# Optimization experiments

Hardware: AMD Instinct MI355X
Metric: run time of the kernel (lower is better)

Reference implementation:

```python
import jax, jax.numpy as jnp
import numpy as np

B, S, D, H, M = 2, 2048, 1024, 16, 4096
DH = D // H
EPS = 1e-6  # flax LayerNorm default
THETA = 10000.0


def layer_norm(x, scale, bias):
    m = jnp.mean(x, axis=-1, keepdims=True)
    v = jnp.var(x, axis=-1, keepdims=True)
    return (x - m) * jax.lax.rsqrt(v + EPS) * scale + bias


def apply_rope(xq, xk):
    # xq, xk: [B, S, H, DH]; rotate consecutive pairs as complex numbers
    half = DH // 2
    freqs = 1.0 / THETA ** (jnp.arange(0, DH, 2)[:half].astype(jnp.float32) / DH)
    t = jnp.arange(S, dtype=jnp.float32)
    ang = jnp.outer(t, freqs)                      # [S, half]
    cos = jnp.cos(ang)[None, :, None, :]           # [1, S, 1, half]
    sin = jnp.sin(ang)[None, :, None, :]

    def rot(x):
        xr = x.astype(jnp.float32).reshape(*x.shape[:-1], half, 2)
        a, b = xr[..., 0], xr[..., 1]
        out = jnp.stack((a * cos - b * sin, a * sin + b * cos), axis=-1)
        return out.reshape(*x.shape).astype(jnp.float32)

    return rot(xq), rot(xk)


def setup_inputs() -> dict:
    key = jax.random.key(0)
    ks = jax.random.split(key, 12)
    sd = 1.0 / np.sqrt(D)
    return {
        "x": jax.random.normal(ks[0], (B, S, D), jnp.float32),
        "ln1_s": jnp.ones((D,), jnp.float32),
        "ln1_b": jnp.zeros((D,), jnp.float32),
        "wk": jax.random.normal(ks[1], (D, D), jnp.float32) * sd,
        "wq": jax.random.normal(ks[2], (D, D), jnp.float32) * sd,
        "wv": jax.random.normal(ks[3], (D, D), jnp.float32) * sd,
        "wo": jax.random.normal(ks[4], (D, D), jnp.float32) * sd,
        "ln2_s": jnp.ones((D,), jnp.float32),
        "ln2_b": jnp.zeros((D,), jnp.float32),
        "w1": jax.random.normal(ks[5], (D, M), jnp.float32) * sd,
        "b1": jnp.zeros((M,), jnp.float32),
        "w2": jax.random.normal(ks[6], (M, D), jnp.float32) * (1.0 / np.sqrt(M)),
        "b2": jnp.zeros((D,), jnp.float32),
    }


def reference(x, ln1_s, ln1_b, wk, wq, wv, wo, ln2_s, ln2_b, w1, b1, w2, b2):
    h = layer_norm(x, ln1_s, ln1_b)
    xk = (h @ wk).reshape(B, S, H, DH)
    xq = (h @ wq).reshape(B, S, H, DH)
    xv = (h @ wv).reshape(B, S, H, DH)
    xq, xk = apply_rope(xq, xk)
    # scores: [B, H, S, S]
    scores = jnp.einsum("bqhd,bkhd->bhqk", xq, xk) / jnp.sqrt(jnp.float32(DH))
    attn = jax.nn.softmax(scores, axis=-1)
    ctx = jnp.einsum("bhqk,bkhd->bqhd", attn, xv).reshape(B, S, D)
    attn_out = ctx @ wo
    mlp_in = attn_out + x
    h2 = layer_norm(mlp_in, ln2_s, ln2_b)
    h2 = jax.nn.gelu(h2 @ w1 + b1)  # approximate gelu (jax default, matches source)
    h2 = h2 @ w2 + b2
    return h2 + mlp_in
```

## Files before the change

kernel.cpp:

```cpp
#include <hip/hip_runtime.h>
#include <stdint.h>

#define B_ 2
#define S_ 2048
#define D_ 1024
#define H_ 16
#define DH_ 64
#define M_ 4096
#define BS_ 4096

typedef __attribute__((ext_vector_type(8))) short short8;
typedef __attribute__((ext_vector_type(4))) float f32x4;
typedef __attribute__((ext_vector_type(16))) float f32x16;

static __device__ __forceinline__ unsigned short f2bf(float f) {
  unsigned u = __float_as_uint(f);
  u += 0x7fffu + ((u >> 16) & 1u);
  return (unsigned short)(u >> 16);
}
static __device__ __forceinline__ float bf2f(unsigned short s) {
  return __uint_as_float(((unsigned)s) << 16);
}
static __device__ __forceinline__ f32x4 MFMA16(short8 a, short8 b, f32x4 c) {
  return __builtin_amdgcn_mfma_f32_16x16x32_bf16(a, b, c, 0, 0, 0);
}
static __device__ __forceinline__ f32x16 MFMA32(short8 a, short8 b, f32x16 c) {
  return __builtin_amdgcn_mfma_f32_32x32x16_bf16(a, b, c, 0, 0, 0);
}
static __device__ __forceinline__ void gload_lds16(const void* g, void* l) {
  __builtin_amdgcn_global_load_lds(
      (const __attribute__((address_space(1))) unsigned int*)g,
      (__attribute__((address_space(3))) unsigned int*)l, 16, 0, 0);
}
static __device__ __forceinline__ unsigned cvtpk_bf16(float lo, float hi) {
  unsigned r;
  asm("v_cvt_pk_bf16_f32 %0, %1, %2" : "=v"(r) : "v"(lo), "v"(hi));
  return r;
}
static __device__ __forceinline__ float gelu_f(float x) {
  float u = 0.7978845608028654f * (x + 0.044715f * x * x * x);
  return 0.5f * x * (1.0f + tanhf(u));
}

__global__ __launch_bounds__(256) void tcast_kernel(const float* __restrict__ in,
                                                    unsigned short* __restrict__ out,
                                                    int R, int C) {
  __shared__ float tile[32][33];
  int tx = threadIdx.x & 31, ty = threadIdx.x >> 5;
  int r0 = blockIdx.y * 32, c0 = blockIdx.x * 32;
#pragma unroll
  for (int i = 0; i < 4; ++i)
    tile[ty + i * 8][tx] = in[(size_t)(r0 + ty + i * 8) * C + c0 + tx];
  __syncthreads();
#pragma unroll
  for (int i = 0; i < 4; ++i)
    out[(size_t)(c0 + ty + i * 8) * R + r0 + tx] = f2bf(tile[tx][ty + i * 8]);
}

__global__ __launch_bounds__(256) void ln_kernel(const float* __restrict__ x,
                                                 const float* __restrict__ sc,
                                                 const float* __restrict__ bi,
                                                 unsigned short* __restrict__ out) {
  int row = blockIdx.x;
  int t = threadIdx.x;
  float4 v = ((const float4*)(x + (size_t)row * D_))[t];
  float s1 = v.x + v.y + v.z + v.w;
  float s2 = v.x * v.x + v.y * v.y + v.z * v.z + v.w * v.w;
#pragma unroll
  for (int m = 1; m < 64; m <<= 1) {
    s1 += __shfl_xor(s1, m);
    s2 += __shfl_xor(s2, m);
  }
  __shared__ float red[8];
  int w = t >> 6, l = t & 63;
  if (l == 0) { red[w] = s1; red[4 + w] = s2; }
  __syncthreads();
  s1 = red[0] + red[1] + red[2] + red[3];
  s2 = red[4] + red[5] + red[6] + red[7];
  float mean = s1 * (1.0f / D_);
  float var = s2 * (1.0f / D_) - mean * mean;
  float rstd = rsqrtf(var + 1e-6f);
  float4 scv = ((const float4*)sc)[t];
  float4 biv = ((const float4*)bi)[t];
  ushort4 o;
  o.x = f2bf((v.x - mean) * rstd * scv.x + biv.x);
  o.y = f2bf((v.y - mean) * rstd * scv.y + biv.y);
  o.z = f2bf((v.z - mean) * rstd * scv.z + biv.z);
  o.w = f2bf((v.w - mean) * rstd * scv.w + biv.w);
  ((ushort4*)out)[(size_t)row * (D_ / 4) + t] = o;
}

__global__ __launch_bounds__(256) void rope_kernel(unsigned short* __restrict__ t_,
                                                   float qscale) {
  size_t idx = (size_t)blockIdx.x * 256 + threadIdx.x;
  int c = (int)(idx & 7);
  size_t rowi = idx >> 3;
  int s = (int)(rowi & (S_ - 1));
  unsigned short* p = t_ + rowi * DH_ + c * 8;
  short8 v = *(const short8*)p;
  unsigned short o[8];
#pragma unroll
  for (int i = 0; i < 4; ++i) {
    int pi = c * 4 + i;
    float freq = exp2f(-(float)pi * 0.4152410118609203f);
    float ang = (float)s * freq;
    float sn, cs;
    sincosf(ang, &sn, &cs);
    float a = bf2f((unsigned short)v[2 * i]);
    float b = bf2f((unsigned short)v[2 * i + 1]);
    o[2 * i] = f2bf((a * cs - b * sn) * qscale);
    o[2 * i + 1] = f2bf((a * sn + b * cs) * qscale);
  }
  short8 ov;
#pragma unroll
  for (int i = 0; i < 8; ++i) ov[i] = (short)o[i];
  *(short8*)p = ov;
}

__global__ __launch_bounds__(256) void attn_kernel(const unsigned short* __restrict__ q,
                                                   const unsigned short* __restrict__ k,
                                                   const unsigned short* __restrict__ vt,
                                                   unsigned short* __restrict__ ctx) {
  __shared__ char smem[49152];
  const int tid = threadIdx.x, w = tid >> 6, l = tid & 63;
  const int lo = l & 31, hi = l >> 5;
  char* Ps = smem + 32768 + w * 4096;
  int flat = blockIdx.y * 16 + blockIdx.x;
  int swz = (flat & 7) * 64 + (flat >> 3);
  const int bh = swz >> 4;
  const int b = bh >> 4, h = bh & 15;
  const int q0 = (swz & 15) * 128 + w * 32;

  const unsigned short* qbase = q + ((size_t)bh * S_ + q0 + lo) * DH_ + hi * 8;
  short8 qf[4];
#pragma unroll
  for (int c = 0; c < 4; ++c) qf[c] = *(const short8*)(qbase + c * 16);

  const unsigned short* kb = k + (size_t)bh * S_ * DH_;
  const unsigned short* vb = vt + (size_t)bh * DH_ * S_;

  short8 onesB;
#pragma unroll
  for (int i = 0; i < 8; ++i) onesB[i] = (short)0x3F80;

  f32x16 o0, o1, lac;
#pragma unroll
  for (int i = 0; i < 16; ++i) { o0[i] = 0.f; o1[i] = 0.f; lac[i] = 0.f; }

#define STAGE_KV(buf, kt)                                                        \
  {                                                                              \
    char* Ks_ = smem + (buf) * 16384;                                            \
    char* Vs_ = Ks_ + 8192;                                                      \
    _Pragma("unroll") for (int i = 0; i < 2; ++i) {                              \
      int slot = i * 256 + tid;                                                  \
      int r = slot >> 3, pc = slot & 7;                                          \
      int sc_ = pc ^ (r & 7);                                                    \
      gload_lds16(kb + (size_t)((kt) + r) * DH_ + sc_ * 8,                       \
                  Ks_ + (i * 4096 + w * 1024));                                  \
      gload_lds16(vb + (size_t)r * S_ + (kt) + sc_ * 8,                          \
                  Vs_ + (i * 4096 + w * 1024));                                  \
    }                                                                            \
  }

  STAGE_KV(0, 0);
  asm volatile("s_waitcnt vmcnt(0)" ::: "memory");
  __builtin_amdgcn_s_barrier();

  for (int t = 0; t < S_ / 64; ++t) {
    int buf = t & 1;
    if (t + 1 < S_ / 64) STAGE_KV(buf ^ 1, (t + 1) * 64);
    char* Ks = smem + buf * 16384;
    char* Vs = Ks + 8192;

#pragma unroll
    for (int kt2 = 0; kt2 < 2; ++kt2) {
      f32x16 z;
#pragma unroll
      for (int i = 0; i < 16; ++i) z[i] = 0.f;
      __builtin_amdgcn_s_setprio(1);
#pragma unroll
      for (int c = 0; c < 4; ++c) {
        int r = kt2 * 32 + lo;
        short8 kf = *(const short8*)(Ks + r * 128 + (((hi + 2 * c) ^ (r & 7)) << 4));
        z = MFMA32(kf, qf[c], z);
      }
      __builtin_amdgcn_s_setprio(0);
      unsigned pk[8];
#pragma unroll
      for (int e = 0; e < 8; ++e)
        pk[e] = cvtpk_bf16(exp2f(z[2 * e]), exp2f(z[2 * e + 1]));
#pragma unroll
      for (int s2 = 0; s2 < 4; ++s2) {
        uint2 dd;
        dd.x = pk[2 * s2];
        dd.y = pk[2 * s2 + 1];
        int slot = kt2 * 4 + s2;
        *(uint2*)(Ps + lo * 128 + ((slot ^ (lo & 7)) << 4) + hi * 8) = dd;
      }
    }

    __builtin_amdgcn_s_setprio(1);
#pragma unroll
    for (int c = 0; c < 4; ++c) {
      short8 pa = *(const short8*)(Ps + lo * 128 + (((2 * c + hi) ^ (lo & 7)) << 4));
      lac = MFMA32(pa, onesB, lac);
      int r0v = lo, r1v = 32 + lo;
      short8 vf0 = *(const short8*)(Vs + r0v * 128 + (((2 * c + hi) ^ (r0v & 7)) << 4));
      short8 vf1 = *(const short8*)(Vs + r1v * 128 + (((2 * c + hi) ^ (r1v & 7)) << 4));
      o0 = MFMA32(pa, vf0, o0);
      o1 = MFMA32(pa, vf1, o1);
    }
    __builtin_amdgcn_s_setprio(0);
    asm volatile("s_waitcnt vmcnt(0)" ::: "memory");
    __builtin_amdgcn_s_barrier();
  }

#pragma unroll
  for (int r = 0; r < 16; ++r) {
    float rl = 1.0f / lac[r];
    int srow = q0 + (r & 3) + 8 * (r >> 2) + 4 * hi;
    unsigned short* cp = ctx + ((size_t)(b * S_) + srow) * D_ + h * DH_ + lo;
    cp[0] = f2bf(o0[r] * rl);
    cp[32] = f2bf(o1[r] * rl);
  }
#undef STAGE_KV
}

template <int EPI, int DBUF>
__global__ __launch_bounds__(256) void gemm_bt(const unsigned short* __restrict__ A,
                                               const unsigned short* __restrict__ Bt,
                                               int K,
                                               const float* __restrict__ aux0,
                                               const float* __restrict__ aux1,
                                               void* __restrict__ out0,
                                               void* __restrict__ out1,
                                               void* __restrict__ out2) {
  __shared__ char smem[DBUF ? 65536 : 32768];
  int tid = threadIdx.x, w = tid >> 6, l = tid & 63;
  int wr = w >> 1, wc = w & 1;
  int gx = gridDim.x;
  int nwg = gx * gridDim.y;
  int flat = blockIdx.y * gx + blockIdx.x;
  int swz = (flat & 7) * (nwg >> 3) + (flat >> 3);
  int row0 = (swz / gx) * 128, col0 = (swz % gx) * 128;
  f32x4 acc[4][4];
#pragma unroll
  for (int mt = 0; mt < 4; ++mt)
#pragma unroll
    for (int nt = 0; nt < 4; ++nt) {
      f32x4 z = {0.f, 0.f, 0.f, 0.f};
      acc[mt][nt] = z;
    }
  int lr = l >> 3, lc = l & 7;

#define STAGE_AB(base, kt)                                                       \
  {                                                                              \
    char* As_ = smem + (base);                                                   \
    char* Bs_ = As_ + 16384;                                                     \
    _Pragma("unroll") for (int i = 0; i < 4; ++i) {                              \
      int rb = w * 32 + i * 8;                                                   \
      int r = rb + lr;                                                           \
      int sc_ = lc ^ (r & 7);                                                    \
      gload_lds16(A + (size_t)(row0 + r) * K + (kt) + sc_ * 8, As_ + rb * 128);  \
      gload_lds16(Bt + (size_t)(col0 + r) * K + (kt) + sc_ * 8, Bs_ + rb * 128); \
    }                                                                            \
  }

#define COMPUTE_STEP(As, Bs)                                                     \
  {                                                                              \
    _Pragma("unroll") for (int kf = 0; kf < 2; ++kf) {                           \
      short8 af[4], bfr[4];                                                      \
      _Pragma("unroll") for (int mt = 0; mt < 4; ++mt) {                         \
        int r = wr * 64 + mt * 16 + (l & 15);                                    \
        int c = (l >> 4) + 4 * kf;                                               \
        af[mt] = *(const short8*)((As) + r * 128 + ((c ^ (r & 7)) << 4));        \
      }                                                                          \
      _Pragma("unroll") for (int nt = 0; nt < 4; ++nt) {                         \
        int r = wc * 64 + nt * 16 + (l & 15);                                    \
        int c = (l >> 4) + 4 * kf;                                               \
        bfr[nt] = *(const short8*)((Bs) + r * 128 + ((c ^ (r & 7)) << 4));       \
      }                                                                          \
      _Pragma("unroll") for (int mt = 0; mt < 4; ++mt)                           \
          _Pragma("unroll") for (int nt = 0; nt < 4; ++nt)                       \
              acc[mt][nt] = MFMA16(af[mt], bfr[nt], acc[mt][nt]);                \
    }                                                                            \
  }

  const int NT = K >> 6;
  if (DBUF) {
    STAGE_AB(0, 0);
    asm volatile("s_waitcnt vmcnt(0)" ::: "memory");
    __builtin_amdgcn_s_barrier();
    for (int t = 0; t < NT; ++t) {
      int buf = t & 1;
      if (t + 1 < NT) STAGE_AB((buf ^ 1) * 32768, (t + 1) * 64);
      char* As = smem + buf * 32768;
      COMPUTE_STEP(As, As + 16384);
      asm volatile("s_waitcnt vmcnt(0)" ::: "memory");
      __builtin_amdgcn_s_barrier();
    }
  } else {
    for (int t = 0; t < NT; ++t) {
      STAGE_AB(0, t * 64);
      __syncthreads();
      COMPUTE_STEP(smem, smem + 16384);
      __syncthreads();
    }
  }
#undef STAGE_AB
#undef COMPUTE_STEP

#pragma unroll
  for (int mt = 0; mt < 4; ++mt) {
#pragma unroll
    for (int nt = 0; nt < 4; ++nt) {
      int grow0 = row0 + wr * 64 + mt * 16 + ((l >> 4) << 2);
      int gcol = col0 + wc * 64 + nt * 16 + (l & 15);
      if (EPI == 0) {
        int which = gcol >> 10;
        int d = gcol & 1023;
        int hh = d >> 6, dh = d & 63;
#pragma unroll
        for (int r = 0; r < 4; ++r) {
          int grow = grow0 + r;
          int b = grow >> 11, s = grow & 2047;
          float v = acc[mt][nt][r];
          if (which == 0)
            ((unsigned short*)out0)[(((size_t)(b * H_ + hh)) * S_ + s) * DH_ + dh] = f2bf(v);
          else if (which == 1)
            ((unsigned short*)out1)[(((size_t)(b * H_ + hh)) * S_ + s) * DH_ + dh] = f2bf(v);
          else
            ((unsigned short*)out2)[(((size_t)(b * H_ + hh)) * DH_ + dh) * S_ + s] = f2bf(v);
        }
      } else if (EPI == 1) {
        float* mo = (float*)out0;
#pragma unroll
        for (int r = 0; r < 4; ++r) {
          int grow = grow0 + r;
          mo[(size_t)grow * D_ + gcol] = acc[mt][nt][r] + aux0[(size_t)grow * D_ + gcol];
        }
      } else if (EPI == 2) {
        unsigned short* gq = (unsigned short*)out0;
        float bb = aux0[gcol];
#pragma unroll
        for (int r = 0; r < 4; ++r) {
          int grow = grow0 + r;
          gq[(size_t)grow * M_ + gcol] = f2bf(gelu_f(acc[mt][nt][r] + bb));
        }
      } else {
        float* po = (float*)out0;
        float bb = aux0[gcol];
#pragma unroll
        for (int r = 0; r < 4; ++r) {
          int grow = grow0 + r;
          po[(size_t)grow * D_ + gcol] =
              acc[mt][nt][r] + bb + aux1[(size_t)grow * D_ + gcol];
        }
      }
    }
  }
}

extern "C" void kernel_launch(void* const* d_in, const int* in_sizes, int n_in,
                              void* d_out, int out_size, void* d_ws, size_t ws_size,
                              hipStream_t stream) {
  const float* x = (const float*)d_in[0];
  const float* ln1s = (const float*)d_in[1];
  const float* ln1b = (const float*)d_in[2];
  const float* wk = (const float*)d_in[3];
  const float* wq = (const float*)d_in[4];
  const float* wv = (const float*)d_in[5];
  const float* wo = (const float*)d_in[6];
  const float* ln2s = (const float*)d_in[7];
  const float* ln2b = (const float*)d_in[8];
  const float* w1 = (const float*)d_in[9];
  const float* b1 = (const float*)d_in[10];
  const float* w2 = (const float*)d_in[11];
  const float* b2 = (const float*)d_in[12];

  char* ws = (char*)d_ws;
  unsigned short* wqkv_t = (unsigned short*)(ws);
  unsigned short* wo_t = (unsigned short*)(ws + 6291456);
  unsigned short* w1_t = (unsigned short*)(ws + 8388608);
  unsigned short* w2_t = (unsigned short*)(ws + 16777216);
  unsigned short* h_bf = (unsigned short*)(ws + 25165824);
  unsigned short* q_bf = (unsigned short*)(ws + 33554432);
  unsigned short* k_bf = (unsigned short*)(ws + 41943040);
  unsigned short* vt_bf = (unsigned short*)(ws + 50331648);
  unsigned short* ctx_bf = (unsigned short*)(ws + 58720256);
  float* mlp_in = (float*)(ws + 67108864);
  unsigned short* g_bf = (unsigned short*)(ws + 83886080);

  dim3 blk(256);
  tcast_kernel<<<dim3(32, 32), blk, 0, stream>>>(wq, wqkv_t, 1024, 1024);
  tcast_kernel<<<dim3(32, 32), blk, 0, stream>>>(wk, wqkv_t + 1048576, 1024, 1024);
  tcast_kernel<<<dim3(32, 32), blk, 0, stream>>>(wv, wqkv_t + 2097152, 1024, 1024);
  tcast_kernel<<<dim3(32, 32), blk, 0, stream>>>(wo, wo_t, 1024, 1024);
  tcast_kernel<<<dim3(128, 32), blk, 0, stream>>>(w1, w1_t, 1024, 4096);
  tcast_kernel<<<dim3(32, 128), blk, 0, stream>>>(w2, w2_t, 4096, 1024);
  ln_kernel<<<dim3(BS_), blk, 0, stream>>>(x, ln1s, ln1b, h_bf);
  gemm_bt<0, 0><<<dim3(24, 32), blk, 0, stream>>>(h_bf, wqkv_t, 1024, nullptr, nullptr,
                                                  q_bf, k_bf, vt_bf);
  rope_kernel<<<dim3(2048), blk, 0, stream>>>(q_bf, 0.125f * 1.4426950408889634f);
  rope_kernel<<<dim3(2048), blk, 0, stream>>>(k_bf, 1.0f);
  attn_kernel<<<dim3(16, 32), blk, 0, stream>>>(q_bf, k_bf, vt_bf, ctx_bf);
  gemm_bt<1, 1><<<dim3(8, 32), blk, 0, stream>>>(ctx_bf, wo_t, 1024, x, nullptr,
                                                 mlp_in, nullptr, nullptr);
  ln_kernel<<<dim3(BS_), blk, 0, stream>>>(mlp_in, ln2s, ln2b, h_bf);
  gemm_bt<2, 0><<<dim3(32, 32), blk, 0, stream>>>(h_bf, w1_t, 1024, b1, nullptr,
                                                  g_bf, nullptr, nullptr);
  gemm_bt<3, 1><<<dim3(8, 32), blk, 0, stream>>>(g_bf, w2_t, 4096, b2, mlp_in,
                                                 (float*)d_out, nullptr, nullptr);
}
```

Measured before the change: 381.5 us.

## Switch all GEMMs to a three-stage LDS ring-buffer pipeline

```diff
diff --git a/kernel.cpp b/kernel.cpp
--- a/kernel.cpp
+++ b/kernel.cpp
@@ -226,16 +226,16 @@
 #undef STAGE_KV
 }
 
-template <int EPI, int DBUF>
-__global__ __launch_bounds__(256) void gemm_bt(const unsigned short* __restrict__ A,
-                                               const unsigned short* __restrict__ Bt,
-                                               int K,
-                                               const float* __restrict__ aux0,
-                                               const float* __restrict__ aux1,
-                                               void* __restrict__ out0,
-                                               void* __restrict__ out1,
-                                               void* __restrict__ out2) {
-  __shared__ char smem[DBUF ? 65536 : 32768];
+template <int EPI>
+__global__ __launch_bounds__(256) void gemm3p(const unsigned short* __restrict__ A,
+                                              const unsigned short* __restrict__ Bt,
+                                              int K,
+                                              const float* __restrict__ aux0,
+                                              const float* __restrict__ aux1,
+                                              void* __restrict__ out0,
+                                              void* __restrict__ out1,
+                                              void* __restrict__ out2) {
+  extern __shared__ char smem[];
   int tid = threadIdx.x, w = tid >> 6, l = tid & 63;
   int wr = w >> 1, wc = w & 1;
   int gx = gridDim.x;
@@ -287,25 +287,21 @@
   }
 
   const int NT = K >> 6;
-  if (DBUF) {
-    STAGE_AB(0, 0);
-    asm volatile("s_waitcnt vmcnt(0)" ::: "memory");
+  STAGE_AB(0, 0);
+  STAGE_AB(32768, 64);
+  int cb = 0;
+  int sb = 2;
+  for (int t = 0; t < NT; ++t) {
+    if (t + 1 < NT)
+      asm volatile("s_waitcnt vmcnt(8)" ::: "memory");
+    else
+      asm volatile("s_waitcnt vmcnt(0)" ::: "memory");
     __builtin_amdgcn_s_barrier();
-    for (int t = 0; t < NT; ++t) {
-      int buf = t & 1;
-      if (t + 1 < NT) STAGE_AB((buf ^ 1) * 32768, (t + 1) * 64);
-      char* As = smem + buf * 32768;
-      COMPUTE_STEP(As, As + 16384);
-      asm volatile("s_waitcnt vmcnt(0)" ::: "memory");
-      __builtin_amdgcn_s_barrier();
-    }
-  } else {
-    for (int t = 0; t < NT; ++t) {
-      STAGE_AB(0, t * 64);
-      __syncthreads();
-      COMPUTE_STEP(smem, smem + 16384);
-      __syncthreads();
-    }
+    if (t + 2 < NT) STAGE_AB(sb * 32768, (t + 2) * 64);
+    char* As = smem + cb * 32768;
+    COMPUTE_STEP(As, As + 16384);
+    cb = (cb == 2) ? 0 : cb + 1;
+    sb = (sb == 2) ? 0 : sb + 1;
   }
 #undef STAGE_AB
 #undef COMPUTE_STEP
@@ -391,6 +387,15 @@
   float* mlp_in = (float*)(ws + 67108864);
   unsigned short* g_bf = (unsigned short*)(ws + 83886080);
 
+  hipFuncSetAttribute((const void*)gemm3p<0>,
+                      hipFuncAttributeMaxDynamicSharedMemorySize, 98304);
+  hipFuncSetAttribute((const void*)gemm3p<1>,
+                      hipFuncAttributeMaxDynamicSharedMemorySize, 98304);
+  hipFuncSetAttribute((const void*)gemm3p<2>,
+                      hipFuncAttributeMaxDynamicSharedMemorySize, 98304);
+  hipFuncSetAttribute((const void*)gemm3p<3>,
+                      hipFuncAttributeMaxDynamicSharedMemorySize, 98304);
+
   dim3 blk(256);
   tcast_kernel<<<dim3(32, 32), blk, 0, stream>>>(wq, wqkv_t, 1024, 1024);
   tcast_kernel<<<dim3(32, 32), blk, 0, stream>>>(wk, wqkv_t + 1048576, 1024, 1024);
@@ -399,16 +404,16 @@
   tcast_kernel<<<dim3(128, 32), blk, 0, stream>>>(w1, w1_t, 1024, 4096);
   tcast_kernel<<<dim3(32, 128), blk, 0, stream>>>(w2, w2_t, 4096, 1024);
   ln_kernel<<<dim3(BS_), blk, 0, stream>>>(x, ln1s, ln1b, h_bf);
-  gemm_bt<0, 0><<<dim3(24, 32), blk, 0, stream>>>(h_bf, wqkv_t, 1024, nullptr, nullptr,
+  gemm3p<0><<<dim3(24, 32), blk, 98304, stream>>>(h_bf, wqkv_t, 1024, nullptr, nullptr,
                                                   q_bf, k_bf, vt_bf);
   rope_kernel<<<dim3(2048), blk, 0, stream>>>(q_bf, 0.125f * 1.4426950408889634f);
   rope_kernel<<<dim3(2048), blk, 0, stream>>>(k_bf, 1.0f);
   attn_kernel<<<dim3(16, 32), blk, 0, stream>>>(q_bf, k_bf, vt_bf, ctx_bf);
-  gemm_bt<1, 1><<<dim3(8, 32), blk, 0, stream>>>(ctx_bf, wo_t, 1024, x, nullptr,
+  gemm3p<1><<<dim3(8, 32), blk, 98304, stream>>>(ctx_bf, wo_t, 1024, x, nullptr,
                                                  mlp_in, nullptr, nullptr);
   ln_kernel<<<dim3(BS_), blk, 0, stream>>>(mlp_in, ln2s, ln2b, h_bf);
-  gemm_bt<2, 0><<<dim3(32, 32), blk, 0, stream>>>(h_bf, w1_t, 1024, b1, nullptr,
+  gemm3p<2><<<dim3(32, 32), blk, 98304, stream>>>(h_bf, w1_t, 1024, b1, nullptr,
                                                   g_bf, nullptr, nullptr);
-  gemm_bt<3, 1><<<dim3(8, 32), blk, 0, stream>>>(g_bf, w2_t, 4096, b2, mlp_in,
+  gemm3p<3><<<dim3(8, 32), blk, 98304, stream>>>(g_bf, w2_t, 4096, b2, mlp_in,
                                                  (float*)d_out, nullptr, nullptr);
 }
```

Result: slower. 415.7 us (+9.0%).

## Double-buffer all GEMMs and remap tiles so each XCD shares A rows

Applied to the files above, without the earlier changes.

```diff
diff --git a/kernel.cpp b/kernel.cpp
--- a/kernel.cpp
+++ b/kernel.cpp
@@ -226,7 +226,7 @@
 #undef STAGE_KV
 }
 
-template <int EPI, int DBUF>
+template <int EPI>
 __global__ __launch_bounds__(256) void gemm_bt(const unsigned short* __restrict__ A,
                                                const unsigned short* __restrict__ Bt,
                                                int K,
@@ -235,14 +235,13 @@
                                                void* __restrict__ out0,
                                                void* __restrict__ out1,
                                                void* __restrict__ out2) {
-  __shared__ char smem[DBUF ? 65536 : 32768];
+  __shared__ char smem[65536];
   int tid = threadIdx.x, w = tid >> 6, l = tid & 63;
   int wr = w >> 1, wc = w & 1;
-  int gx = gridDim.x;
-  int nwg = gx * gridDim.y;
-  int flat = blockIdx.y * gx + blockIdx.x;
-  int swz = (flat & 7) * (nwg >> 3) + (flat >> 3);
-  int row0 = (swz / gx) * 128, col0 = (swz % gx) * 128;
+  int flat = blockIdx.y * gridDim.x + blockIdx.x;
+  int xcd = flat & 7, j = flat >> 3;
+  int row0 = (xcd * 4 + (j & 3)) * 128;
+  int col0 = (j >> 2) * 128;
   f32x4 acc[4][4];
 #pragma unroll
   for (int mt = 0; mt < 4; ++mt)
@@ -287,25 +286,16 @@
   }
 
   const int NT = K >> 6;
-  if (DBUF) {
-    STAGE_AB(0, 0);
+  STAGE_AB(0, 0);
+  asm volatile("s_waitcnt vmcnt(0)" ::: "memory");
+  __builtin_amdgcn_s_barrier();
+  for (int t = 0; t < NT; ++t) {
+    int buf = t & 1;
+    if (t + 1 < NT) STAGE_AB((buf ^ 1) * 32768, (t + 1) * 64);
+    char* As = smem + buf * 32768;
+    COMPUTE_STEP(As, As + 16384);
     asm volatile("s_waitcnt vmcnt(0)" ::: "memory");
     __builtin_amdgcn_s_barrier();
-    for (int t = 0; t < NT; ++t) {
-      int buf = t & 1;
-      if (t + 1 < NT) STAGE_AB((buf ^ 1) * 32768, (t + 1) * 64);
-      char* As = smem + buf * 32768;
-      COMPUTE_STEP(As, As + 16384);
-      asm volatile("s_waitcnt vmcnt(0)" ::: "memory");
-      __builtin_amdgcn_s_barrier();
-    }
-  } else {
-    for (int t = 0; t < NT; ++t) {
-      STAGE_AB(0, t * 64);
-      __syncthreads();
-      COMPUTE_STEP(smem, smem + 16384);
-      __syncthreads();
-    }
   }
 #undef STAGE_AB
 #undef COMPUTE_STEP
@@ -399,16 +389,16 @@
   tcast_kernel<<<dim3(128, 32), blk, 0, stream>>>(w1, w1_t, 1024, 4096);
   tcast_kernel<<<dim3(32, 128), blk, 0, stream>>>(w2, w2_t, 4096, 1024);
   ln_kernel<<<dim3(BS_), blk, 0, stream>>>(x, ln1s, ln1b, h_bf);
-  gemm_bt<0, 0><<<dim3(24, 32), blk, 0, stream>>>(h_bf, wqkv_t, 1024, nullptr, nullptr,
-                                                  q_bf, k_bf, vt_bf);
+  gemm_bt<0><<<dim3(24, 32), blk, 0, stream>>>(h_bf, wqkv_t, 1024, nullptr, nullptr,
+                                               q_bf, k_bf, vt_bf);
   rope_kernel<<<dim3(2048), blk, 0, stream>>>(q_bf, 0.125f * 1.4426950408889634f);
   rope_kernel<<<dim3(2048), blk, 0, stream>>>(k_bf, 1.0f);
   attn_kernel<<<dim3(16, 32), blk, 0, stream>>>(q_bf, k_bf, vt_bf, ctx_bf);
-  gemm_bt<1, 1><<<dim3(8, 32), blk, 0, stream>>>(ctx_bf, wo_t, 1024, x, nullptr,
-                                                 mlp_in, nullptr, nullptr);
+  gemm_bt<1><<<dim3(8, 32), blk, 0, stream>>>(ctx_bf, wo_t, 1024, x, nullptr,
+                                              mlp_in, nullptr, nullptr);
   ln_kernel<<<dim3(BS_), blk, 0, stream>>>(mlp_in, ln2s, ln2b, h_bf);
-  gemm_bt<2, 0><<<dim3(32, 32), blk, 0, stream>>>(h_bf, w1_t, 1024, b1, nullptr,
-                                                  g_bf, nullptr, nullptr);
-  gemm_bt<3, 1><<<dim3(8, 32), blk, 0, stream>>>(g_bf, w2_t, 4096, b2, mlp_in,
-                                                 (float*)d_out, nullptr, nullptr);
-}
+  gemm_bt<2><<<dim3(32, 32), blk, 0, stream>>>(h_bf, w1_t, 1024, b1, nullptr,
+                                               g_bf, nullptr, nullptr);
+  gemm_bt<3><<<dim3(8, 32), blk, 0, stream>>>(g_bf, w2_t, 4096, b2, mlp_in,
+                                              (float*)d_out, nullptr, nullptr);
+}
```

Measured after the change: 373.8 us. -2.0%, faster.
